# Optimization experiments

Hardware: AMD Instinct MI355X
Metric: run time of the kernel (lower is better)

The kernel has to match this reference:

```python
import jax, jax.numpy as jnp
import numpy as np

N, E, H, L = 20000, 1_280_000, 64, 4


def setup_inputs() -> dict:
    key = jax.random.key(0)
    ks = jax.random.split(key, 24)
    inputs = jax.random.normal(ks[0], (1, N, 6), jnp.float32)
    node_masks = jnp.ones((1, N), jnp.int32)
    send_edges = jax.random.randint(ks[1], (E,), 0, N)
    recv_edges = jax.random.randint(ks[2], (E,), 0, N)

    def w(k, shape, scale=None):
        s = (1.0 / np.sqrt(shape[-2])) if scale is None else scale
        return (jax.random.normal(k, shape, jnp.float32) * s)

    d = dict(
        inputs=inputs, node_masks=node_masks,
        send_edges=send_edges, recv_edges=recv_edges,
        emb_w=w(ks[3], (1, H)), emb_b=jnp.zeros((H,), jnp.float32),
        edge_w1=w(ks[4], (L, 2 * H + 1, H)), edge_b1=jnp.zeros((L, H), jnp.float32),
        edge_w2=w(ks[5], (L, H, H)), edge_b2=jnp.zeros((L, H), jnp.float32),
        node_w1=w(ks[6], (L, 2 * H, H)), node_b1=jnp.zeros((L, H), jnp.float32),
        node_w2=w(ks[7], (L, H, H)), node_b2=jnp.zeros((L, H), jnp.float32),
        coord_w1=w(ks[8], (L, H, H)), coord_b1=jnp.zeros((L, H), jnp.float32),
        coord_wout=w(ks[9], (L, H, 1), scale=0.001),  # xavier gain=0.001, no bias
        vel_w1=w(ks[10], (L, H, H)), vel_b1=jnp.zeros((L, H), jnp.float32),
        vel_w2=w(ks[11], (L, H, 1)), vel_b2=jnp.zeros((L, 1), jnp.float32),
    )
    return d


def reference(inputs, node_masks, send_edges, recv_edges,
              emb_w, emb_b, edge_w1, edge_b1, edge_w2, edge_b2,
              node_w1, node_b1, node_w2, node_b2,
              coord_w1, coord_b1, coord_wout,
              vel_w1, vel_b1, vel_w2, vel_b2):
    silu = jax.nn.silu
    # node_masks is all-ones -> node_inds = arange(N); all nodes active.
    pos, vel = jnp.split(inputs, 2, axis=-1)          # [1,N,3] each
    h = jnp.linalg.norm(vel, axis=-1, keepdims=True)  # speed -> [1,N,1]
    h = h @ emb_w + emb_b                             # [1,N,H]
    coord = pos
    n = coord.shape[1]
    counts = jax.ops.segment_sum(jnp.ones_like(recv_edges, dtype=coord.dtype),
                                 recv_edges, num_segments=n)
    inv_cnt = (1.0 / jnp.maximum(counts, 1.0))[None, :, None]
    seg = lambda e: jax.ops.segment_sum(e, recv_edges, num_segments=n)

    for l in range(L):
        # coord2radial
        cd = coord[:, send_edges] - coord[:, recv_edges]        # [1,E,3]
        radial = jnp.sum(cd * cd, -1, keepdims=True)            # [1,E,1]
        # edge_model
        ef_in = jnp.concatenate([h[:, send_edges], h[:, recv_edges], radial], -1)
        ef = silu(silu(ef_in @ edge_w1[l] + edge_b1[l]) @ edge_w2[l] + edge_b2[l])
        # coord_model
        cm = silu(ef @ coord_w1[l] + coord_b1[l]) @ coord_wout[l]  # [1,E,1]
        trans = jnp.clip(cd * cm, -100.0, 100.0)
        agg_mean = jax.vmap(seg)(trans) * inv_cnt                  # scatter_mean
        # velocity update
        v_gate = silu(h @ vel_w1[l] + vel_b1[l]) @ vel_w2[l] + vel_b2[l]
        vel = agg_mean + v_gate * vel
        coord = coord + vel
        # node_model (recurrent residual)
        agg_sum = jax.vmap(seg)(ef)                                # scatter_sum
        hn = jnp.concatenate([h, agg_sum], -1)
        h = silu(hn @ node_w1[l] + node_b1[l]) @ node_w2[l] + node_b2[l] + h

    pred = jnp.concatenate([coord, vel], -1)  # [1,N,6] == pred_all (all active)
    return pred
```

## Files before the change

kernel.cpp:

```cpp
#include <hip/hip_runtime.h>
#include <math.h>

#define N_NODES 20000
#define N_EDGES 1280000
#define NLAYERS 4
#define NTILE (N_EDGES/32)
#define TSTRIDE 68
#define SCHUNK 79

typedef short bf16x8 __attribute__((ext_vector_type(8)));
typedef float f32x4  __attribute__((ext_vector_type(4)));
typedef long long i64;
typedef unsigned short us;

__device__ __forceinline__ float silu_f(float x) {
    return x * __builtin_amdgcn_rcpf(1.0f + __expf(-x));
}

__device__ __forceinline__ us f2b(float x) {
    union { float f; unsigned u; } v; v.f = x;
    unsigned r = v.u + 0x7FFF + ((v.u >> 16) & 1);
    return (us)(r >> 16);
}
__device__ __forceinline__ float b2f(us u) {
    union { float f; unsigned u; } v; v.u = ((unsigned)u) << 16;
    return v.f;
}
__device__ __forceinline__ void split2r(float x, us& hi, us& lo) {
    hi = f2b(x);
    lo = f2b(x - b2f(hi));
}
__device__ __forceinline__ void split2f(float x, us& hi, us& lo) {
    union { float f; unsigned u; } v; v.f = x;
    hi = (us)(v.u >> 16);
    union { float f; unsigned u; } h; h.u = v.u & 0xFFFF0000u;
    union { float f; unsigned u; } r; r.f = x - h.f;
    lo = (us)(r.u >> 16);
}

__device__ __forceinline__ bf16x8 ld8(const us* p) {
    bf16x8 a;
    ((i64*)&a)[0] = *(const i64*)p;
    ((i64*)&a)[1] = *(const i64*)(p + 4);
    return a;
}

__device__ __forceinline__ void mfma3(f32x4& acc, bf16x8 ahi, bf16x8 alo,
                                      bf16x8 bhi, bf16x8 blo) {
    acc = __builtin_amdgcn_mfma_f32_16x16x32_bf16(ahi, bhi, acc, 0, 0, 0);
    acc = __builtin_amdgcn_mfma_f32_16x16x32_bf16(alo, bhi, acc, 0, 0, 0);
    acc = __builtin_amdgcn_mfma_f32_16x16x32_bf16(ahi, blo, acc, 0, 0, 0);
}

__global__ void k_init(const float* __restrict__ inp,
                       const float* __restrict__ emb_w,
                       const float* __restrict__ emb_b,
                       float* __restrict__ outv,
                       us* __restrict__ hbh, us* __restrict__ hbl) {
    int t = blockIdx.x * blockDim.x + threadIdx.x;
    int n = t >> 6, f = t & 63;
    if (n >= N_NODES) return;
    float vx = inp[n*6+3], vy = inp[n*6+4], vz = inp[n*6+5];
    float sp = sqrtf(vx*vx + vy*vy + vz*vz);
    float hv = sp * emb_w[f] + emb_b[f];
    us hi, lo; split2r(hv, hi, lo);
    hbh[t] = hi; hbl[t] = lo;
    if (f < 6) outv[n*6+f] = inp[n*6+f];
}

__global__ void k_cnt(const int* __restrict__ recv, int* __restrict__ counts) {
    int t = blockIdx.x*256 + threadIdx.x;
    if (t < N_EDGES) atomicAdd(&counts[recv[t]], 1);
}

__global__ void k_scan(const int* __restrict__ counts, int* __restrict__ rowstart,
                       int* __restrict__ cursor, int* __restrict__ tile2node) {
    __shared__ int buf[256];
    const int tid = threadIdx.x;
    const int lo = tid*SCHUNK;
    const int hi = (lo + SCHUNK < N_NODES) ? lo + SCHUNK : N_NODES;
    int s = 0;
    for (int i = lo; i < hi; ++i) s += counts[i];
    buf[tid] = s;
    __syncthreads();
    for (int off = 1; off < 256; off <<= 1) {
        int v = (tid >= off) ? buf[tid-off] : 0;
        __syncthreads();
        buf[tid] += v;
        __syncthreads();
    }
    int run = buf[tid] - s;
    for (int i = lo; i < hi; ++i) {
        rowstart[i] = run; cursor[i] = run;
        const int c = counts[i];
        for (int t = (run + 31) >> 5; t*32 < run + c; ++t) tile2node[t] = i;
        run += c;
    }
    if (tid < 20) rowstart[N_NODES + tid] = N_EDGES;
}

__global__ void k_scatter(const int* __restrict__ send, const int* __restrict__ recv,
                          int* __restrict__ cursor, us* __restrict__ sp16) {
    int t = blockIdx.x*256 + threadIdx.x;
    if (t < N_EDGES) {
        int p = atomicAdd(&cursor[recv[t]], 1);
        sp16[p] = (us)send[t];
    }
}

__global__ void k_prepw(const float* __restrict__ ew1, const float* __restrict__ ew2,
                        const float* __restrict__ cw1,
                        us* __restrict__ w1th, us* __restrict__ w1tl,
                        us* __restrict__ w2th, us* __restrict__ w2tl,
                        us* __restrict__ cw1th, us* __restrict__ cw1tl) {
    int t = blockIdx.x*256 + threadIdx.x;
    int l = t >> 14;
    int r = t & 16383;
    us hi, lo;
    if (r < 8192) {
        int n = r >> 7, k = r & 127;
        split2r(ew1[l*129*64 + k*64 + n], hi, lo);
        w1th[l*8192 + r] = hi; w1tl[l*8192 + r] = lo;
    } else if (r < 12288) {
        int rr = r - 8192; int n = rr >> 6, k = rr & 63;
        split2r(ew2[l*4096 + k*64 + n], hi, lo);
        w2th[l*4096 + n*64 + k] = hi; w2tl[l*4096 + n*64 + k] = lo;
    } else {
        int rr = r - 12288; int n = rr >> 6, k = rr & 63;
        split2r(cw1[l*4096 + k*64 + n], hi, lo);
        cw1th[l*4096 + n*64 + k] = hi; cw1tl[l*4096 + n*64 + k] = lo;
    }
}

__launch_bounds__(256, 4)
__global__ void k_recv(const us* __restrict__ hbh, const us* __restrict__ hbl,
                       const float* __restrict__ ew1,
                       const float* __restrict__ eb1,
                       float* __restrict__ R) {
    __shared__ float hs[4][64];
    const int tid = threadIdx.x;
    const int nn = tid >> 6, f = tid & 63;
    const int n = blockIdx.x*4 + nn;
    hs[nn][f] = b2f(hbh[(size_t)n*64+f]) + b2f(hbl[(size_t)n*64+f]);
    __syncthreads();
    float s = eb1[f];
    for (int k = 0; k < 64; ++k) s += hs[nn][k] * ew1[(64+k)*64 + f];
    R[(size_t)n*64+f] = s;
}

__launch_bounds__(128, 4)
__global__ void k_edge(const us* __restrict__ sp16, const int* __restrict__ rowstart,
                       const int* __restrict__ tile2node,
                       const us* __restrict__ hbh, const us* __restrict__ hbl,
                       const float* __restrict__ outv,
                       const float* __restrict__ R,
                       const us* __restrict__ w1th, const us* __restrict__ w1tl,
                       const us* __restrict__ w2th, const us* __restrict__ w2tl,
                       const us* __restrict__ cw1th, const us* __restrict__ cw1tl,
                       const float* __restrict__ ew1,
                       const float* __restrict__ eb2, const float* __restrict__ cb1,
                       const float* __restrict__ cwo,
                       float* __restrict__ aggs, float* __restrict__ aggm) {
    __shared__ us tileh[2][32*TSTRIDE];
    __shared__ us tilel[2][32*TSTRIDE];

    const int tid  = threadIdx.x;
    const int wid  = tid >> 6;
    const int lane = tid & 63;
    const int q    = lane >> 4;
    const int l15  = lane & 15;
    const int wbase = blockIdx.x*64 + wid*32;
    const int wtile = blockIdx.x*2 + wid;

    const int e0 = wbase + l15, e1 = e0 + 16;
    const int s0 = sp16[e0], s1 = sp16[e1];

    const int t2n = tile2node[wtile];
    const int wv = rowstart[t2n + 1 + l15];
    int seg0 = 0, seg1 = 0;
    #pragma unroll
    for (int i = 0; i < 16; ++i) {
        const int wi = __shfl(wv, i);
        seg0 += (e0 >= wi);
        seg1 += (e1 >= wi);
    }
    const int r0 = t2n + seg0, r1 = t2n + seg1;

    int sgrow[2][4];
    #pragma unroll
    for (int r = 0; r < 4; ++r) {
        sgrow[0][r] = __shfl(seg0, 4*q + r);
        sgrow[1][r] = __shfl(seg1, 4*q + r);
    }
    const int segA = __shfl(seg0, 0);
    const int segB = __shfl(seg1, 15);

    const float cdx0 = outv[s0*6+0]-outv[r0*6+0], cdy0 = outv[s0*6+1]-outv[r0*6+1], cdz0 = outv[s0*6+2]-outv[r0*6+2];
    const float cdx1 = outv[s1*6+0]-outv[r1*6+0], cdy1 = outv[s1*6+1]-outv[r1*6+1], cdz1 = outv[s1*6+2]-outv[r1*6+2];
    const float rad0 = cdx0*cdx0+cdy0*cdy0+cdz0*cdz0;
    const float rad1 = cdx1*cdx1+cdy1*cdy1+cdz1*cdz1;

    f32x4 acc[2][4];

    if (segB == segA) {
        const int rn = t2n + segA;
        #pragma unroll
        for (int t = 0; t < 4; ++t) {
            const float rv = R[(size_t)rn*64 + 16*t + l15];
            #pragma unroll
            for (int mu = 0; mu < 2; ++mu)
                #pragma unroll
                for (int r = 0; r < 4; ++r) acc[mu][t][r] = rv;
        }
    } else {
        #pragma unroll
        for (int mu = 0; mu < 2; ++mu)
            #pragma unroll
            for (int r = 0; r < 4; ++r) {
                const size_t ro = (size_t)(t2n + sgrow[mu][r])*64;
                #pragma unroll
                for (int t = 0; t < 4; ++t)
                    acc[mu][t][r] = R[ro + 16*t + l15];
            }
    }

    #pragma unroll
    for (int kc = 0; kc < 2; ++kc) {
        const int off = kc*32 + q*8;
        const size_t o0 = (size_t)s0*64 + off;
        const size_t o1 = (size_t)s1*64 + off;
        bf16x8 a0h = ld8(hbh + o0), a0l = ld8(hbl + o0);
        bf16x8 a1h = ld8(hbh + o1), a1l = ld8(hbl + o1);
        #pragma unroll
        for (int t = 0; t < 4; ++t) {
            const int wo = (16*t + l15)*128 + off;
            bf16x8 bh = ld8(w1th + wo), bl = ld8(w1tl + wo);
            mfma3(acc[0][t], a0h, a0l, bh, bl);
            mfma3(acc[1][t], a1h, a1l, bh, bl);
        }
    }

    float rsh0[4], rsh1[4];
    #pragma unroll
    for (int r = 0; r < 4; ++r) {
        rsh0[r] = __shfl(rad0, 4*q + r);
        rsh1[r] = __shfl(rad1, 4*q + r);
    }
    #pragma unroll
    for (int t = 0; t < 4; ++t) {
        const float wl = ew1[128*64 + 16*t + l15];
        #pragma unroll
        for (int r = 0; r < 4; ++r) {
            acc[0][t][r] += rsh0[r]*wl;
            acc[1][t][r] += rsh1[r]*wl;
        }
    }

    us* Th = tileh[wid];
    us* Tl = tilel[wid];
    #pragma unroll
    for (int mu = 0; mu < 2; ++mu)
        #pragma unroll
        for (int t = 0; t < 4; ++t)
            #pragma unroll
            for (int r = 0; r < 4; ++r) {
                us hi, lo; split2f(silu_f(acc[mu][t][r]), hi, lo);
                const int ti = (mu*16 + 4*q + r)*TSTRIDE + 16*t + l15;
                Th[ti] = hi; Tl[ti] = lo;
            }
    __asm__ volatile("s_waitcnt lgkmcnt(0)" ::: "memory");

    #pragma unroll
    for (int mu = 0; mu < 2; ++mu)
        #pragma unroll
        for (int t = 0; t < 4; ++t) acc[mu][t] = (f32x4){0.f,0.f,0.f,0.f};
    #pragma unroll
    for (int kc = 0; kc < 2; ++kc) {
        const int t0 = l15*TSTRIDE + kc*32 + q*8;
        const int t1i = (16+l15)*TSTRIDE + kc*32 + q*8;
        bf16x8 a0h = ld8(Th + t0),  a0l = ld8(Tl + t0);
        bf16x8 a1h = ld8(Th + t1i), a1l = ld8(Tl + t1i);
        #pragma unroll
        for (int t = 0; t < 4; ++t) {
            const int wo = (16*t + l15)*64 + kc*32 + q*8;
            bf16x8 bh = ld8(w2th + wo), bl = ld8(w2tl + wo);
            mfma3(acc[0][t], a0h, a0l, bh, bl);
            mfma3(acc[1][t], a1h, a1l, bh, bl);
        }
    }

    float ef[2][4][4];
    #pragma unroll
    for (int t = 0; t < 4; ++t) {
        const float bb = eb2[16*t + l15];
        #pragma unroll
        for (int mu = 0; mu < 2; ++mu)
            #pragma unroll
            for (int r = 0; r < 4; ++r)
                ef[mu][t][r] = silu_f(acc[mu][t][r] + bb);
    }
    __asm__ volatile("s_waitcnt lgkmcnt(0)" ::: "memory");
    #pragma unroll
    for (int mu = 0; mu < 2; ++mu)
        #pragma unroll
        for (int t = 0; t < 4; ++t)
            #pragma unroll
            for (int r = 0; r < 4; ++r) {
                us hi, lo; split2f(ef[mu][t][r], hi, lo);
                const int ti = (mu*16 + 4*q + r)*TSTRIDE + 16*t + l15;
                Th[ti] = hi; Tl[ti] = lo;
            }
    __asm__ volatile("s_waitcnt lgkmcnt(0)" ::: "memory");

    #pragma unroll
    for (int mu = 0; mu < 2; ++mu)
        #pragma unroll
        for (int t = 0; t < 4; ++t) acc[mu][t] = (f32x4){0.f,0.f,0.f,0.f};
    #pragma unroll
    for (int kc = 0; kc < 2; ++kc) {
        const int t0 = l15*TSTRIDE + kc*32 + q*8;
        const int t1i = (16+l15)*TSTRIDE + kc*32 + q*8;
        bf16x8 a0h = ld8(Th + t0),  a0l = ld8(Tl + t0);
        bf16x8 a1h = ld8(Th + t1i), a1l = ld8(Tl + t1i);
        #pragma unroll
        for (int t = 0; t < 4; ++t) {
            const int wo = (16*t + l15)*64 + kc*32 + q*8;
            bf16x8 bh = ld8(cw1th + wo), bl = ld8(cw1tl + wo);
            mfma3(acc[0][t], a0h, a0l, bh, bl);
            mfma3(acc[1][t], a1h, a1l, bh, bl);
        }
    }

    float cm0[4] = {0.f,0.f,0.f,0.f}, cm1[4] = {0.f,0.f,0.f,0.f};
    #pragma unroll
    for (int t = 0; t < 4; ++t) {
        const int col = 16*t + l15;
        const float cb = cb1[col];
        const float co = cwo[col];
        #pragma unroll
        for (int r = 0; r < 4; ++r) {
            cm0[r] += silu_f(acc[0][t][r] + cb) * co;
            cm1[r] += silu_f(acc[1][t][r] + cb) * co;
        }
    }
    #pragma unroll
    for (int m = 1; m <= 8; m <<= 1)
        #pragma unroll
        for (int r = 0; r < 4; ++r) {
            cm0[r] += __shfl_xor(cm0[r], m);
            cm1[r] += __shfl_xor(cm1[r], m);
        }

    float tv[2][4];
    #pragma unroll
    for (int mu = 0; mu < 2; ++mu)
        #pragma unroll
        for (int r = 0; r < 4; ++r) {
            const float cxv = __shfl(mu ? cdx1 : cdx0, 4*q + r);
            const float cyv = __shfl(mu ? cdy1 : cdy0, 4*q + r);
            const float czv = __shfl(mu ? cdz1 : cdz0, 4*q + r);
            const float cmv = mu ? cm1[r] : cm0[r];
            const float sel = (l15 == 0) ? cxv : (l15 == 1) ? cyv : czv;
            tv[mu][r] = (l15 < 3) ? fminf(fmaxf(sel*cmv, -100.f), 100.f) : 0.f;
        }

    if (segB == segA) {
        float s4[4], trT = 0.f;
        #pragma unroll
        for (int t = 0; t < 4; ++t) {
            float v = 0.f;
            #pragma unroll
            for (int mu = 0; mu < 2; ++mu)
                #pragma unroll
                for (int r = 0; r < 4; ++r) v += ef[mu][t][r];
            v += __shfl_xor(v, 16);
            v += __shfl_xor(v, 32);
            s4[t] = v;
        }
        #pragma unroll
        for (int mu = 0; mu < 2; ++mu)
            #pragma unroll
            for (int r = 0; r < 4; ++r) trT += tv[mu][r];
        trT += __shfl_xor(trT, 16);
        trT += __shfl_xor(trT, 32);
        const int rn = t2n + segA;
        if (q == 0) {
            #pragma unroll
            for (int t = 0; t < 4; ++t)
                atomicAdd(&aggs[(size_t)rn*64 + 16*t + l15], s4[t]);
            if (l15 < 3) atomicAdd(&aggm[rn*3 + l15], trT);
        }
    } else if (segB == segA + 1) {
        float sA[4] = {0,0,0,0}, sB[4] = {0,0,0,0};
        float trA = 0.f, trB = 0.f;
        #pragma unroll
        for (int mu = 0; mu < 2; ++mu)
            #pragma unroll
            for (int r = 0; r < 4; ++r) {
                const bool isA = (sgrow[mu][r] == segA);
                #pragma unroll
                for (int t = 0; t < 4; ++t) {
                    const float v = ef[mu][t][r];
                    sA[t] += isA ? v : 0.f;
                    sB[t] += isA ? 0.f : v;
                }
                const float tvv = tv[mu][r];
                trA += isA ? tvv : 0.f;
                trB += isA ? 0.f : tvv;
            }
        #pragma unroll
        for (int t = 0; t < 4; ++t) {
            sA[t] += __shfl_xor(sA[t], 16); sA[t] += __shfl_xor(sA[t], 32);
            sB[t] += __shfl_xor(sB[t], 16); sB[t] += __shfl_xor(sB[t], 32);
        }
        trA += __shfl_xor(trA, 16); trA += __shfl_xor(trA, 32);
        trB += __shfl_xor(trB, 16); trB += __shfl_xor(trB, 32);
        const int rnA = t2n + segA, rnB = rnA + 1;
        if (q == 0) {
            #pragma unroll
            for (int t = 0; t < 4; ++t) {
                atomicAdd(&aggs[(size_t)rnA*64 + 16*t + l15], sA[t]);
                atomicAdd(&aggs[(size_t)rnB*64 + 16*t + l15], sB[t]);
            }
            if (l15 < 3) {
                atomicAdd(&aggm[rnA*3 + l15], trA);
                atomicAdd(&aggm[rnB*3 + l15], trB);
            }
        }
    } else {
        #pragma unroll
        for (int mu = 0; mu < 2; ++mu)
            #pragma unroll
            for (int r = 0; r < 4; ++r) {
                const int ren = t2n + sgrow[mu][r];
                #pragma unroll
                for (int t = 0; t < 4; ++t)
                    atomicAdd(&aggs[(size_t)ren*64 + 16*t + l15], ef[mu][t][r]);
                if (l15 < 3) atomicAdd(&aggm[ren*3 + l15], tv[mu][r]);
            }
    }
}

__launch_bounds__(256, 4)
__global__ void k_node(float* __restrict__ aggs, float* __restrict__ aggm,
                       const int* __restrict__ rowstart,
                       const float* __restrict__ VW1, const float* __restrict__ vb1,
                       const float* __restrict__ VW2, const float* __restrict__ vb2,
                       const float* __restrict__ NW1, const float* __restrict__ nb1,
                       const float* __restrict__ NW2, const float* __restrict__ nb2,
                       float* __restrict__ outv,
                       us* __restrict__ hbh, us* __restrict__ hbl,
                       const float* __restrict__ EW1n,
                       const float* __restrict__ eb1n,
                       float* __restrict__ R, int doR) {
    __shared__ float hs[4][64], as[4][64], tt[4][64];
    const int tid = threadIdx.x;
    const int nn = tid >> 6, f = tid & 63;
    const int n = blockIdx.x*4 + nn;
    float hv = b2f(hbh[n*64+f]) + b2f(hbl[n*64+f]);
    hs[nn][f] = hv;
    as[nn][f] = aggs[n*64+f];
    aggs[n*64+f] = 0.f;
    __syncthreads();

    float a1 = vb1[f];
    for (int k = 0; k < 64; ++k) a1 += hs[nn][k] * VW1[k*64+f];
    float p = silu_f(a1) * VW2[f];
    #pragma unroll
    for (int o = 32; o > 0; o >>= 1) p += __shfl_down(p, o);
    float vgate = __shfl(p, 0) + vb2[0];

    if (f < 3) {
        float icnt = 1.0f / fmaxf((float)(rowstart[n+1] - rowstart[n]), 1.0f);
        float nv = aggm[n*3+f]*icnt + vgate*outv[n*6+3+f];
        aggm[n*3+f] = 0.f;
        outv[n*6+3+f] = nv;
        outv[n*6+f]  += nv;
    }

    float b = nb1[f];
    for (int k = 0; k < 64; ++k) b += hs[nn][k]*NW1[k*64+f];
    for (int k = 0; k < 64; ++k) b += as[nn][k]*NW1[(64+k)*64+f];
    __syncthreads();
    tt[nn][f] = silu_f(b);
    __syncthreads();
    float o = nb2[f] + hv;
    for (int k = 0; k < 64; ++k) o += tt[nn][k]*NW2[k*64+f];
    us hi, lo; split2r(o, hi, lo);
    hbh[n*64+f] = hi; hbl[n*64+f] = lo;

    if (doR) {
        hs[nn][f] = o;
        __syncthreads();
        float s = eb1n[f];
        for (int k = 0; k < 64; ++k) s += hs[nn][k] * EW1n[(64+k)*64 + f];
        R[(size_t)n*64+f] = s;
    }
}

extern "C" void kernel_launch(void* const* d_in, const int* in_sizes, int n_in,
                              void* d_out, int out_size, void* d_ws, size_t ws_size,
                              hipStream_t stream) {
    const float* inp   = (const float*)d_in[0];
    const int*   send  = (const int*)d_in[2];
    const int*   recv  = (const int*)d_in[3];
    const float* emb_w = (const float*)d_in[4];
    const float* emb_b = (const float*)d_in[5];
    const float* ew1   = (const float*)d_in[6];
    const float* eb1   = (const float*)d_in[7];
    const float* ew2   = (const float*)d_in[8];
    const float* eb2   = (const float*)d_in[9];
    const float* nw1   = (const float*)d_in[10];
    const float* nb1   = (const float*)d_in[11];
    const float* nw2   = (const float*)d_in[12];
    const float* nb2   = (const float*)d_in[13];
    const float* cw1   = (const float*)d_in[14];
    const float* cb1   = (const float*)d_in[15];
    const float* cwo   = (const float*)d_in[16];
    const float* vw1   = (const float*)d_in[17];
    const float* vb1   = (const float*)d_in[18];
    const float* vw2   = (const float*)d_in[19];
    const float* vb2   = (const float*)d_in[20];

    float* outv = (float*)d_out;

    float* ws        = (float*)d_ws;
    float* aggs      = ws;
    float* aggm      = aggs + (size_t)N_NODES*64;
    int*   rowstart  = (int*)(aggm + N_NODES*3);
    int*   tile2node = rowstart + (N_NODES+20);
    us*    hbh       = (us*)(tile2node + NTILE);
    us*    hbl       = hbh + (size_t)N_NODES*64;
    us*    sp16      = hbl + (size_t)N_NODES*64;
    us*    w1th      = sp16 + N_EDGES;
    us*    w1tl      = w1th + 4*8192;
    us*    w2th      = w1tl + 4*8192;
    us*    w2tl      = w2th + 4*4096;
    us*    cw1th     = w2tl + 4*4096;
    us*    cw1tl     = cw1th + 4*4096;
    float* R         = (float*)(cw1tl + 4*4096);
    int*   counts    = (int*)aggs;
    int*   cursor    = counts + N_NODES;

    hipMemsetAsync(counts, 0, N_NODES*sizeof(int), stream);
    k_init<<<(N_NODES*64)/256, 256, 0, stream>>>(inp, emb_w, emb_b, outv, hbh, hbl);
    k_cnt<<<(N_EDGES+255)/256, 256, 0, stream>>>(recv, counts);
    k_scan<<<1, 256, 0, stream>>>(counts, rowstart, cursor, tile2node);
    k_scatter<<<(N_EDGES+255)/256, 256, 0, stream>>>(send, recv, cursor, sp16);
    k_prepw<<<256, 256, 0, stream>>>(ew1, ew2, cw1, w1th, w1tl, w2th, w2tl, cw1th, cw1tl);
    hipMemsetAsync(aggs, 0, (size_t)N_NODES*67*sizeof(float), stream);
    k_recv<<<N_NODES/4, 256, 0, stream>>>(hbh, hbl, ew1, eb1, R);

    for (int l = 0; l < NLAYERS; ++l) {
        k_edge<<<N_EDGES/64, 128, 0, stream>>>(sp16, rowstart, tile2node, hbh, hbl, outv, R,
            w1th + l*8192, w1tl + l*8192,
            w2th + l*4096, w2tl + l*4096,
            cw1th + l*4096, cw1tl + l*4096,
            ew1 + (size_t)l*129*64, eb2 + l*64,
            cb1 + l*64, cwo + l*64,
            aggs, aggm);
        const int doR = (l < NLAYERS-1);
        k_node<<<N_NODES/4, 256, 0, stream>>>(aggs, aggm, rowstart,
            vw1 + (size_t)l*64*64, vb1 + l*64, vw2 + l*64, vb2 + l,
            nw1 + (size_t)l*128*64, nb1 + l*64,
            nw2 + (size_t)l*64*64,  nb2 + l*64,
            outv, hbh, hbl,
            ew1 + (size_t)(l+1 < NLAYERS ? l+1 : l)*129*64,
            eb1 + (l+1 < NLAYERS ? l+1 : l)*64,
            R, doR);
    }
}
```

Baseline: 1.777 ms.

## Swap MFMA operand roles to chain edge MLP layers in registers without LDS

```diff
diff --git a/kernel.cpp b/kernel.cpp
--- a/kernel.cpp
+++ b/kernel.cpp
@@ -5,7 +5,6 @@
 #define N_EDGES 1280000
 #define NLAYERS 4
 #define NTILE (N_EDGES/32)
-#define TSTRIDE 68
 #define SCHUNK 79
 
 typedef short bf16x8 __attribute__((ext_vector_type(8)));
@@ -43,6 +42,16 @@
     ((i64*)&a)[0] = *(const i64*)p;
     ((i64*)&a)[1] = *(const i64*)(p + 4);
     return a;
+}
+
+__device__ __forceinline__ bf16x8 pack8(us h0, us h1, us h2, us h3,
+                                        us l0, us l1, us l2, us l3) {
+    union { bf16x8 v; unsigned u[4]; } w;
+    w.u[0] = (unsigned)h0 | ((unsigned)h1 << 16);
+    w.u[1] = (unsigned)h2 | ((unsigned)h3 << 16);
+    w.u[2] = (unsigned)l0 | ((unsigned)l1 << 16);
+    w.u[3] = (unsigned)l2 | ((unsigned)l3 << 16);
+    return w.v;
 }
 
 __device__ __forceinline__ void mfma3(f32x4& acc, bf16x8 ahi, bf16x8 alo,
@@ -111,24 +120,30 @@
 __global__ void k_prepw(const float* __restrict__ ew1, const float* __restrict__ ew2,
                         const float* __restrict__ cw1,
                         us* __restrict__ w1th, us* __restrict__ w1tl,
-                        us* __restrict__ w2th, us* __restrict__ w2tl,
-                        us* __restrict__ cw1th, us* __restrict__ cw1tl) {
+                        us* __restrict__ w2a1, us* __restrict__ w2a2,
+                        us* __restrict__ cwa1, us* __restrict__ cwa2) {
     int t = blockIdx.x*256 + threadIdx.x;
-    int l = t >> 14;
-    int r = t & 16383;
+    int l = t / 24576;
+    int r = t % 24576;
     us hi, lo;
     if (r < 8192) {
         int n = r >> 7, k = r & 127;
         split2r(ew1[l*129*64 + k*64 + n], hi, lo);
         w1th[l*8192 + r] = hi; w1tl[l*8192 + r] = lo;
-    } else if (r < 12288) {
-        int rr = r - 8192; int n = rr >> 6, k = rr & 63;
-        split2r(ew2[l*4096 + k*64 + n], hi, lo);
-        w2th[l*4096 + n*64 + k] = hi; w2tl[l*4096 + n*64 + k] = lo;
+    } else if (r < 16384) {
+        int rr = r - 8192;
+        int m = rr >> 7, v = rr & 127;
+        int kt = v >> 5, qq = (v >> 3) & 3, j = v & 7;
+        int f = 16*kt + 4*qq + (j & 3);
+        split2r(ew2[l*4096 + f*64 + m], hi, lo);
+        w2a1[l*8192 + rr] = hi; w2a2[l*8192 + rr] = lo;
     } else {
-        int rr = r - 12288; int n = rr >> 6, k = rr & 63;
-        split2r(cw1[l*4096 + k*64 + n], hi, lo);
-        cw1th[l*4096 + n*64 + k] = hi; cw1tl[l*4096 + n*64 + k] = lo;
+        int rr = r - 16384;
+        int m = rr >> 7, v = rr & 127;
+        int kt = v >> 5, qq = (v >> 3) & 3, j = v & 7;
+        int f = 16*kt + 4*qq + (j & 3);
+        split2r(cw1[l*4096 + f*64 + m], hi, lo);
+        cwa1[l*8192 + rr] = hi; cwa2[l*8192 + rr] = lo;
     }
 }
 
@@ -143,9 +158,14 @@
     const int n = blockIdx.x*4 + nn;
     hs[nn][f] = b2f(hbh[(size_t)n*64+f]) + b2f(hbl[(size_t)n*64+f]);
     __syncthreads();
-    float s = eb1[f];
-    for (int k = 0; k < 64; ++k) s += hs[nn][k] * ew1[(64+k)*64 + f];
-    R[(size_t)n*64+f] = s;
+    float p0 = 0.f, p1 = 0.f, p2 = 0.f, p3 = 0.f;
+    for (int k = 0; k < 64; k += 4) {
+        p0 += hs[nn][k+0] * ew1[(64+k+0)*64 + f];
+        p1 += hs[nn][k+1] * ew1[(64+k+1)*64 + f];
+        p2 += hs[nn][k+2] * ew1[(64+k+2)*64 + f];
+        p3 += hs[nn][k+3] * ew1[(64+k+3)*64 + f];
+    }
+    R[(size_t)n*64+f] = eb1[f] + (p0+p1) + (p2+p3);
 }
 
 __launch_bounds__(128, 4)
@@ -155,20 +175,18 @@
                        const float* __restrict__ outv,
                        const float* __restrict__ R,
                        const us* __restrict__ w1th, const us* __restrict__ w1tl,
-                       const us* __restrict__ w2th, const us* __restrict__ w2tl,
-                       const us* __restrict__ cw1th, const us* __restrict__ cw1tl,
+                       const us* __restrict__ w2a1, const us* __restrict__ w2a2,
+                       const us* __restrict__ cwa1, const us* __restrict__ cwa2,
                        const float* __restrict__ ew1,
                        const float* __restrict__ eb2, const float* __restrict__ cb1,
                        const float* __restrict__ cwo,
                        float* __restrict__ aggs, float* __restrict__ aggm) {
-    __shared__ us tileh[2][32*TSTRIDE];
-    __shared__ us tilel[2][32*TSTRIDE];
-
     const int tid  = threadIdx.x;
     const int wid  = tid >> 6;
     const int lane = tid & 63;
     const int q    = lane >> 4;
     const int l15  = lane & 15;
+    const int q8   = q*8, qb = q*4;
     const int wbase = blockIdx.x*64 + wid*32;
     const int wtile = blockIdx.x*2 + wid;
 
@@ -185,13 +203,6 @@
         seg1 += (e1 >= wi);
     }
     const int r0 = t2n + seg0, r1 = t2n + seg1;
-
-    int sgrow[2][4];
-    #pragma unroll
-    for (int r = 0; r < 4; ++r) {
-        sgrow[0][r] = __shfl(seg0, 4*q + r);
-        sgrow[1][r] = __shfl(seg1, 4*q + r);
-    }
     const int segA = __shfl(seg0, 0);
     const int segB = __shfl(seg1, 15);
 
@@ -200,244 +211,217 @@
     const float rad0 = cdx0*cdx0+cdy0*cdy0+cdz0*cdz0;
     const float rad1 = cdx1*cdx1+cdy1*cdy1+cdz1*cdz1;
 
+    f32x4 wl4[4], eb24[4], cb14[4], cwo4[4];
+    #pragma unroll
+    for (int t = 0; t < 4; ++t) {
+        const int cb = 16*t + qb;
+        wl4[t]  = *(const f32x4*)&ew1[8192 + cb];
+        eb24[t] = *(const f32x4*)&eb2[cb];
+        cb14[t] = *(const f32x4*)&cb1[cb];
+        cwo4[t] = *(const f32x4*)&cwo[cb];
+    }
+
     f32x4 acc[2][4];
-
     if (segB == segA) {
         const int rn = t2n + segA;
         #pragma unroll
         for (int t = 0; t < 4; ++t) {
-            const float rv = R[(size_t)rn*64 + 16*t + l15];
-            #pragma unroll
-            for (int mu = 0; mu < 2; ++mu)
-                #pragma unroll
-                for (int r = 0; r < 4; ++r) acc[mu][t][r] = rv;
+            const f32x4 rv = *(const f32x4*)&R[(size_t)rn*64 + 16*t + qb];
+            acc[0][t] = rv; acc[1][t] = rv;
         }
     } else {
-        #pragma unroll
-        for (int mu = 0; mu < 2; ++mu)
-            #pragma unroll
-            for (int r = 0; r < 4; ++r) {
-                const size_t ro = (size_t)(t2n + sgrow[mu][r])*64;
-                #pragma unroll
-                for (int t = 0; t < 4; ++t)
-                    acc[mu][t][r] = R[ro + 16*t + l15];
-            }
+        const size_t o0 = (size_t)(t2n + seg0)*64;
+        const size_t o1 = (size_t)(t2n + seg1)*64;
+        #pragma unroll
+        for (int t = 0; t < 4; ++t) {
+            acc[0][t] = *(const f32x4*)&R[o0 + 16*t + qb];
+            acc[1][t] = *(const f32x4*)&R[o1 + 16*t + qb];
+        }
     }
 
     #pragma unroll
     for (int kc = 0; kc < 2; ++kc) {
-        const int off = kc*32 + q*8;
-        const size_t o0 = (size_t)s0*64 + off;
-        const size_t o1 = (size_t)s1*64 + off;
-        bf16x8 a0h = ld8(hbh + o0), a0l = ld8(hbl + o0);
-        bf16x8 a1h = ld8(hbh + o1), a1l = ld8(hbl + o1);
+        const int off = kc*32 + q8;
+        bf16x8 b0h = ld8(hbh + (size_t)s0*64 + off), b0l = ld8(hbl + (size_t)s0*64 + off);
+        bf16x8 b1h = ld8(hbh + (size_t)s1*64 + off), b1l = ld8(hbl + (size_t)s1*64 + off);
         #pragma unroll
         for (int t = 0; t < 4; ++t) {
             const int wo = (16*t + l15)*128 + off;
-            bf16x8 bh = ld8(w1th + wo), bl = ld8(w1tl + wo);
-            mfma3(acc[0][t], a0h, a0l, bh, bl);
-            mfma3(acc[1][t], a1h, a1l, bh, bl);
-        }
-    }
-
-    float rsh0[4], rsh1[4];
-    #pragma unroll
-    for (int r = 0; r < 4; ++r) {
-        rsh0[r] = __shfl(rad0, 4*q + r);
-        rsh1[r] = __shfl(rad1, 4*q + r);
-    }
-    #pragma unroll
-    for (int t = 0; t < 4; ++t) {
-        const float wl = ew1[128*64 + 16*t + l15];
+            bf16x8 ah = ld8(w1th + wo), al = ld8(w1tl + wo);
+            mfma3(acc[0][t], ah, al, b0h, b0l);
+            mfma3(acc[1][t], ah, al, b1h, b1l);
+        }
+    }
+
+    #pragma unroll
+    for (int t = 0; t < 4; ++t)
         #pragma unroll
         for (int r = 0; r < 4; ++r) {
-            acc[0][t][r] += rsh0[r]*wl;
-            acc[1][t][r] += rsh1[r]*wl;
-        }
-    }
-
-    us* Th = tileh[wid];
-    us* Tl = tilel[wid];
+            acc[0][t][r] += rad0 * wl4[t][r];
+            acc[1][t][r] += rad1 * wl4[t][r];
+        }
+
+    f32x4 acc2[2][4];
     #pragma unroll
     for (int mu = 0; mu < 2; ++mu)
         #pragma unroll
+        for (int t = 0; t < 4; ++t) acc2[mu][t] = (f32x4){0.f,0.f,0.f,0.f};
+    #pragma unroll
+    for (int mu = 0; mu < 2; ++mu)
+        #pragma unroll
+        for (int kt = 0; kt < 4; ++kt) {
+            us h0,h1,h2,h3,l0,l1,l2,l3;
+            split2f(silu_f(acc[mu][kt][0]), h0, l0);
+            split2f(silu_f(acc[mu][kt][1]), h1, l1);
+            split2f(silu_f(acc[mu][kt][2]), h2, l2);
+            split2f(silu_f(acc[mu][kt][3]), h3, l3);
+            const bf16x8 B = pack8(h0,h1,h2,h3, l0,l1,l2,l3);
+            #pragma unroll
+            for (int t = 0; t < 4; ++t) {
+                const int wo = (16*t + l15)*128 + kt*32 + q8;
+                bf16x8 a1 = ld8(w2a1 + wo), a2 = ld8(w2a2 + wo);
+                acc2[mu][t] = __builtin_amdgcn_mfma_f32_16x16x32_bf16(a1, B, acc2[mu][t], 0, 0, 0);
+                acc2[mu][t] = __builtin_amdgcn_mfma_f32_16x16x32_bf16(a2, B, acc2[mu][t], 0, 0, 0);
+            }
+        }
+
+    f32x4 ef[2][4];
+    #pragma unroll
+    for (int mu = 0; mu < 2; ++mu)
+        #pragma unroll
         for (int t = 0; t < 4; ++t)
             #pragma unroll
+            for (int r = 0; r < 4; ++r)
+                ef[mu][t][r] = silu_f(acc2[mu][t][r] + eb24[t][r]);
+
+    f32x4 acc3[2][4];
+    #pragma unroll
+    for (int mu = 0; mu < 2; ++mu)
+        #pragma unroll
+        for (int t = 0; t < 4; ++t) acc3[mu][t] = (f32x4){0.f,0.f,0.f,0.f};
+    #pragma unroll
+    for (int mu = 0; mu < 2; ++mu)
+        #pragma unroll
+        for (int kt = 0; kt < 4; ++kt) {
+            us h0,h1,h2,h3,l0,l1,l2,l3;
+            split2f(ef[mu][kt][0], h0, l0);
+            split2f(ef[mu][kt][1], h1, l1);
+            split2f(ef[mu][kt][2], h2, l2);
+            split2f(ef[mu][kt][3], h3, l3);
+            const bf16x8 B = pack8(h0,h1,h2,h3, l0,l1,l2,l3);
+            #pragma unroll
+            for (int t = 0; t < 4; ++t) {
+                const int wo = (16*t + l15)*128 + kt*32 + q8;
+                bf16x8 a1 = ld8(cwa1 + wo), a2 = ld8(cwa2 + wo);
+                acc3[mu][t] = __builtin_amdgcn_mfma_f32_16x16x32_bf16(a1, B, acc3[mu][t], 0, 0, 0);
+                acc3[mu][t] = __builtin_amdgcn_mfma_f32_16x16x32_bf16(a2, B, acc3[mu][t], 0, 0, 0);
+            }
+        }
+
+    float cmv0 = 0.f, cmv1 = 0.f;
+    #pragma unroll
+    for (int t = 0; t < 4; ++t)
+        #pragma unroll
+        for (int r = 0; r < 4; ++r) {
+            cmv0 += silu_f(acc3[0][t][r] + cb14[t][r]) * cwo4[t][r];
+            cmv1 += silu_f(acc3[1][t][r] + cb14[t][r]) * cwo4[t][r];
+        }
+    cmv0 += __shfl_xor(cmv0, 16); cmv0 += __shfl_xor(cmv0, 32);
+    cmv1 += __shfl_xor(cmv1, 16); cmv1 += __shfl_xor(cmv1, 32);
+
+    float tv[2][3];
+    tv[0][0] = fminf(fmaxf(cdx0*cmv0, -100.f), 100.f);
+    tv[0][1] = fminf(fmaxf(cdy0*cmv0, -100.f), 100.f);
+    tv[0][2] = fminf(fmaxf(cdz0*cmv0, -100.f), 100.f);
+    tv[1][0] = fminf(fmaxf(cdx1*cmv1, -100.f), 100.f);
+    tv[1][1] = fminf(fmaxf(cdy1*cmv1, -100.f), 100.f);
+    tv[1][2] = fminf(fmaxf(cdz1*cmv1, -100.f), 100.f);
+
+    if (segB == segA) {
+        f32x4 v[4];
+        #pragma unroll
+        for (int t = 0; t < 4; ++t) {
+            v[t] = ef[0][t] + ef[1][t];
+            #pragma unroll
             for (int r = 0; r < 4; ++r) {
-                us hi, lo; split2f(silu_f(acc[mu][t][r]), hi, lo);
-                const int ti = (mu*16 + 4*q + r)*TSTRIDE + 16*t + l15;
-                Th[ti] = hi; Tl[ti] = lo;
+                float x = v[t][r];
+                x += __shfl_xor(x, 1); x += __shfl_xor(x, 2);
+                x += __shfl_xor(x, 4); x += __shfl_xor(x, 8);
+                v[t][r] = x;
             }
-    __asm__ volatile("s_waitcnt lgkmcnt(0)" ::: "memory");
-
-    #pragma unroll
-    for (int mu = 0; mu < 2; ++mu)
-        #pragma unroll
-        for (int t = 0; t < 4; ++t) acc[mu][t] = (f32x4){0.f,0.f,0.f,0.f};
-    #pragma unroll
-    for (int kc = 0; kc < 2; ++kc) {
-        const int t0 = l15*TSTRIDE + kc*32 + q*8;
-        const int t1i = (16+l15)*TSTRIDE + kc*32 + q*8;
-        bf16x8 a0h = ld8(Th + t0),  a0l = ld8(Tl + t0);
-        bf16x8 a1h = ld8(Th + t1i), a1l = ld8(Tl + t1i);
+        }
+        float t0 = tv[0][0]+tv[1][0], t1 = tv[0][1]+tv[1][1], t2 = tv[0][2]+tv[1][2];
+        t0 += __shfl_xor(t0,1); t0 += __shfl_xor(t0,2); t0 += __shfl_xor(t0,4); t0 += __shfl_xor(t0,8);
+        t1 += __shfl_xor(t1,1); t1 += __shfl_xor(t1,2); t1 += __shfl_xor(t1,4); t1 += __shfl_xor(t1,8);
+        t2 += __shfl_xor(t2,1); t2 += __shfl_xor(t2,2); t2 += __shfl_xor(t2,4); t2 += __shfl_xor(t2,8);
+        const int rn = t2n + segA;
+        if (l15 == 0) {
+            #pragma unroll
+            for (int t = 0; t < 4; ++t)
+                #pragma unroll
+                for (int r = 0; r < 4; ++r)
+                    atomicAdd(&aggs[(size_t)rn*64 + 16*t + qb + r], v[t][r]);
+        }
+        if (q == 0 && l15 < 3) {
+            const float w = (l15 == 0) ? t0 : (l15 == 1) ? t1 : t2;
+            atomicAdd(&aggm[rn*3 + l15], w);
+        }
+    } else if (segB == segA + 1) {
+        const bool A0 = (seg0 == segA), A1 = (seg1 == segA);
+        f32x4 vA[4], vB[4];
         #pragma unroll
         for (int t = 0; t < 4; ++t) {
-            const int wo = (16*t + l15)*64 + kc*32 + q*8;
-            bf16x8 bh = ld8(w2th + wo), bl = ld8(w2tl + wo);
-            mfma3(acc[0][t], a0h, a0l, bh, bl);
-            mfma3(acc[1][t], a1h, a1l, bh, bl);
-        }
-    }
-
-    float ef[2][4][4];
-    #pragma unroll
-    for (int t = 0; t < 4; ++t) {
-        const float bb = eb2[16*t + l15];
-        #pragma unroll
-        for (int mu = 0; mu < 2; ++mu)
-            #pragma unroll
-            for (int r = 0; r < 4; ++r)
-                ef[mu][t][r] = silu_f(acc[mu][t][r] + bb);
-    }
-    __asm__ volatile("s_waitcnt lgkmcnt(0)" ::: "memory");
-    #pragma unroll
-    for (int mu = 0; mu < 2; ++mu)
+            #pragma unroll
+            for (int r = 0; r < 4; ++r) {
+                const float a = (A0 ? ef[0][t][r] : 0.f) + (A1 ? ef[1][t][r] : 0.f);
+                const float b = (A0 ? 0.f : ef[0][t][r]) + (A1 ? 0.f : ef[1][t][r]);
+                float xa = a, xb = b;
+                xa += __shfl_xor(xa,1); xa += __shfl_xor(xa,2); xa += __shfl_xor(xa,4); xa += __shfl_xor(xa,8);
+                xb += __shfl_xor(xb,1); xb += __shfl_xor(xb,2); xb += __shfl_xor(xb,4); xb += __shfl_xor(xb,8);
+                vA[t][r] = xa; vB[t][r] = xb;
+            }
+        }
+        float trA[3], trB[3];
+        #pragma unroll
+        for (int c = 0; c < 3; ++c) {
+            float a = (A0 ? tv[0][c] : 0.f) + (A1 ? tv[1][c] : 0.f);
+            float b = (A0 ? 0.f : tv[0][c]) + (A1 ? 0.f : tv[1][c]);
+            a += __shfl_xor(a,1); a += __shfl_xor(a,2); a += __shfl_xor(a,4); a += __shfl_xor(a,8);
+            b += __shfl_xor(b,1); b += __shfl_xor(b,2); b += __shfl_xor(b,4); b += __shfl_xor(b,8);
+            trA[c] = a; trB[c] = b;
+        }
+        const int rnA = t2n + segA, rnB = rnA + 1;
+        if (l15 == 0) {
+            #pragma unroll
+            for (int t = 0; t < 4; ++t)
+                #pragma unroll
+                for (int r = 0; r < 4; ++r) {
+                    atomicAdd(&aggs[(size_t)rnA*64 + 16*t + qb + r], vA[t][r]);
+                    atomicAdd(&aggs[(size_t)rnB*64 + 16*t + qb + r], vB[t][r]);
+                }
+        }
+        if (q == 0 && l15 < 3) {
+            const float wa = (l15 == 0) ? trA[0] : (l15 == 1) ? trA[1] : trA[2];
+            const float wb = (l15 == 0) ? trB[0] : (l15 == 1) ? trB[1] : trB[2];
+            atomicAdd(&aggm[rnA*3 + l15], wa);
+            atomicAdd(&aggm[rnB*3 + l15], wb);
+        }
+    } else {
+        const int n0 = t2n + seg0, n1 = t2n + seg1;
         #pragma unroll
         for (int t = 0; t < 4; ++t)
             #pragma unroll
             for (int r = 0; r < 4; ++r) {
-                us hi, lo; split2f(ef[mu][t][r], hi, lo);
-                const int ti = (mu*16 + 4*q + r)*TSTRIDE + 16*t + l15;
-                Th[ti] = hi; Tl[ti] = lo;
+                atomicAdd(&aggs[(size_t)n0*64 + 16*t + qb + r], ef[0][t][r]);
+                atomicAdd(&aggs[(size_t)n1*64 + 16*t + qb + r], ef[1][t][r]);
             }
-    __asm__ volatile("s_waitcnt lgkmcnt(0)" ::: "memory");
-
-    #pragma unroll
-    for (int mu = 0; mu < 2; ++mu)
-        #pragma unroll
-        for (int t = 0; t < 4; ++t) acc[mu][t] = (f32x4){0.f,0.f,0.f,0.f};
-    #pragma unroll
-    for (int kc = 0; kc < 2; ++kc) {
-        const int t0 = l15*TSTRIDE + kc*32 + q*8;
-        const int t1i = (16+l15)*TSTRIDE + kc*32 + q*8;
-        bf16x8 a0h = ld8(Th + t0),  a0l = ld8(Tl + t0);
-        bf16x8 a1h = ld8(Th + t1i), a1l = ld8(Tl + t1i);
-        #pragma unroll
-        for (int t = 0; t < 4; ++t) {
-            const int wo = (16*t + l15)*64 + kc*32 + q*8;
-            bf16x8 bh = ld8(cw1th + wo), bl = ld8(cw1tl + wo);
-            mfma3(acc[0][t], a0h, a0l, bh, bl);
-            mfma3(acc[1][t], a1h, a1l, bh, bl);
-        }
-    }
-
-    float cm0[4] = {0.f,0.f,0.f,0.f}, cm1[4] = {0.f,0.f,0.f,0.f};
-    #pragma unroll
-    for (int t = 0; t < 4; ++t) {
-        const int col = 16*t + l15;
-        const float cb = cb1[col];
-        const float co = cwo[col];
-        #pragma unroll
-        for (int r = 0; r < 4; ++r) {
-            cm0[r] += silu_f(acc[0][t][r] + cb) * co;
-            cm1[r] += silu_f(acc[1][t][r] + cb) * co;
-        }
-    }
-    #pragma unroll
-    for (int m = 1; m <= 8; m <<= 1)
-        #pragma unroll
-        for (int r = 0; r < 4; ++r) {
-            cm0[r] += __shfl_xor(cm0[r], m);
-            cm1[r] += __shfl_xor(cm1[r], m);
-        }
-
-    float tv[2][4];
-    #pragma unroll
-    for (int mu = 0; mu < 2; ++mu)
-        #pragma unroll
-        for (int r = 0; r < 4; ++r) {
-            const float cxv = __shfl(mu ? cdx1 : cdx0, 4*q + r);
-            const float cyv = __shfl(mu ? cdy1 : cdy0, 4*q + r);
-            const float czv = __shfl(mu ? cdz1 : cdz0, 4*q + r);
-            const float cmv = mu ? cm1[r] : cm0[r];
-            const float sel = (l15 == 0) ? cxv : (l15 == 1) ? cyv : czv;
-            tv[mu][r] = (l15 < 3) ? fminf(fmaxf(sel*cmv, -100.f), 100.f) : 0.f;
-        }
-
-    if (segB == segA) {
-        float s4[4], trT = 0.f;
-        #pragma unroll
-        for (int t = 0; t < 4; ++t) {
-            float v = 0.f;
-            #pragma unroll
-            for (int mu = 0; mu < 2; ++mu)
-                #pragma unroll
-                for (int r = 0; r < 4; ++r) v += ef[mu][t][r];
-            v += __shfl_xor(v, 16);
-            v += __shfl_xor(v, 32);
-            s4[t] = v;
-        }
-        #pragma unroll
-        for (int mu = 0; mu < 2; ++mu)
-            #pragma unroll
-            for (int r = 0; r < 4; ++r) trT += tv[mu][r];
-        trT += __shfl_xor(trT, 16);
-        trT += __shfl_xor(trT, 32);
-        const int rn = t2n + segA;
         if (q == 0) {
             #pragma unroll
-            for (int t = 0; t < 4; ++t)
-                atomicAdd(&aggs[(size_t)rn*64 + 16*t + l15], s4[t]);
-            if (l15 < 3) atomicAdd(&aggm[rn*3 + l15], trT);
-        }
-    } else if (segB == segA + 1) {
-        float sA[4] = {0,0,0,0}, sB[4] = {0,0,0,0};
-        float trA = 0.f, trB = 0.f;
-        #pragma unroll
-        for (int mu = 0; mu < 2; ++mu)
-            #pragma unroll
-            for (int r = 0; r < 4; ++r) {
-                const bool isA = (sgrow[mu][r] == segA);
-                #pragma unroll
-                for (int t = 0; t < 4; ++t) {
-                    const float v = ef[mu][t][r];
-                    sA[t] += isA ? v : 0.f;
-                    sB[t] += isA ? 0.f : v;
-                }
-                const float tvv = tv[mu][r];
-                trA += isA ? tvv : 0.f;
-                trB += isA ? 0.f : tvv;
+            for (int c = 0; c < 3; ++c) {
+                atomicAdd(&aggm[n0*3 + c], tv[0][c]);
+                atomicAdd(&aggm[n1*3 + c], tv[1][c]);
             }
-        #pragma unroll
-        for (int t = 0; t < 4; ++t) {
-            sA[t] += __shfl_xor(sA[t], 16); sA[t] += __shfl_xor(sA[t], 32);
-            sB[t] += __shfl_xor(sB[t], 16); sB[t] += __shfl_xor(sB[t], 32);
-        }
-        trA += __shfl_xor(trA, 16); trA += __shfl_xor(trA, 32);
-        trB += __shfl_xor(trB, 16); trB += __shfl_xor(trB, 32);
-        const int rnA = t2n + segA, rnB = rnA + 1;
-        if (q == 0) {
-            #pragma unroll
-            for (int t = 0; t < 4; ++t) {
-                atomicAdd(&aggs[(size_t)rnA*64 + 16*t + l15], sA[t]);
-                atomicAdd(&aggs[(size_t)rnB*64 + 16*t + l15], sB[t]);
-            }
-            if (l15 < 3) {
-                atomicAdd(&aggm[rnA*3 + l15], trA);
-                atomicAdd(&aggm[rnB*3 + l15], trB);
-            }
-        }
-    } else {
-        #pragma unroll
-        for (int mu = 0; mu < 2; ++mu)
-            #pragma unroll
-            for (int r = 0; r < 4; ++r) {
-                const int ren = t2n + sgrow[mu][r];
-                #pragma unroll
-                for (int t = 0; t < 4; ++t)
-                    atomicAdd(&aggs[(size_t)ren*64 + 16*t + l15], ef[mu][t][r]);
-                if (l15 < 3) atomicAdd(&aggm[ren*3 + l15], tv[mu][r]);
-            }
+        }
     }
 }
 
@@ -463,8 +447,15 @@
     aggs[n*64+f] = 0.f;
     __syncthreads();
 
-    float a1 = vb1[f];
-    for (int k = 0; k < 64; ++k) a1 += hs[nn][k] * VW1[k*64+f];
+    float p0, p1, p2, p3;
+    p0 = p1 = p2 = p3 = 0.f;
+    for (int k = 0; k < 64; k += 4) {
+        p0 += hs[nn][k+0] * VW1[(k+0)*64+f];
+        p1 += hs[nn][k+1] * VW1[(k+1)*64+f];
+        p2 += hs[nn][k+2] * VW1[(k+2)*64+f];
+        p3 += hs[nn][k+3] * VW1[(k+3)*64+f];
+    }
+    float a1 = vb1[f] + (p0+p1) + (p2+p3);
     float p = silu_f(a1) * VW2[f];
     #pragma unroll
     for (int o = 32; o > 0; o >>= 1) p += __shfl_down(p, o);
@@ -478,23 +469,39 @@
         outv[n*6+f]  += nv;
     }
 
-    float b = nb1[f];
-    for (int k = 0; k < 64; ++k) b += hs[nn][k]*NW1[k*64+f];
-    for (int k = 0; k < 64; ++k) b += as[nn][k]*NW1[(64+k)*64+f];
+    p0 = p1 = p2 = p3 = 0.f;
+    for (int k = 0; k < 64; k += 4) {
+        p0 += hs[nn][k+0]*NW1[(k+0)*64+f] + as[nn][k+0]*NW1[(64+k+0)*64+f];
+        p1 += hs[nn][k+1]*NW1[(k+1)*64+f] + as[nn][k+1]*NW1[(64+k+1)*64+f];
+        p2 += hs[nn][k+2]*NW1[(k+2)*64+f] + as[nn][k+2]*NW1[(64+k+2)*64+f];
+        p3 += hs[nn][k+3]*NW1[(k+3)*64+f] + as[nn][k+3]*NW1[(64+k+3)*64+f];
+    }
+    float b = nb1[f] + (p0+p1) + (p2+p3);
     __syncthreads();
     tt[nn][f] = silu_f(b);
     __syncthreads();
-    float o = nb2[f] + hv;
-    for (int k = 0; k < 64; ++k) o += tt[nn][k]*NW2[k*64+f];
+    p0 = p1 = p2 = p3 = 0.f;
+    for (int k = 0; k < 64; k += 4) {
+        p0 += tt[nn][k+0]*NW2[(k+0)*64+f];
+        p1 += tt[nn][k+1]*NW2[(k+1)*64+f];
+        p2 += tt[nn][k+2]*NW2[(k+2)*64+f];
+        p3 += tt[nn][k+3]*NW2[(k+3)*64+f];
+    }
+    float o = nb2[f] + hv + (p0+p1) + (p2+p3);
     us hi, lo; split2r(o, hi, lo);
     hbh[n*64+f] = hi; hbl[n*64+f] = lo;
 
     if (doR) {
         hs[nn][f] = o;
         __syncthreads();
-        float s = eb1n[f];
-        for (int k = 0; k < 64; ++k) s += hs[nn][k] * EW1n[(64+k)*64 + f];
-        R[(size_t)n*64+f] = s;
+        p0 = p1 = p2 = p3 = 0.f;
+        for (int k = 0; k < 64; k += 4) {
+            p0 += hs[nn][k+0] * EW1n[(64+k+0)*64 + f];
+            p1 += hs[nn][k+1] * EW1n[(64+k+1)*64 + f];
+            p2 += hs[nn][k+2] * EW1n[(64+k+2)*64 + f];
+            p3 += hs[nn][k+3] * EW1n[(64+k+3)*64 + f];
+        }
+        R[(size_t)n*64+f] = eb1n[f] + (p0+p1) + (p2+p3);
     }
 }
 
@@ -534,11 +541,11 @@
     us*    sp16      = hbl + (size_t)N_NODES*64;
     us*    w1th      = sp16 + N_EDGES;
     us*    w1tl      = w1th + 4*8192;
-    us*    w2th      = w1tl + 4*8192;
-    us*    w2tl      = w2th + 4*4096;
-    us*    cw1th     = w2tl + 4*4096;
-    us*    cw1tl     = cw1th + 4*4096;
-    float* R         = (float*)(cw1tl + 4*4096);
+    us*    w2a1      = w1tl + 4*8192;
+    us*    w2a2      = w2a1 + 4*8192;
+    us*    cwa1      = w2a2 + 4*8192;
+    us*    cwa2      = cwa1 + 4*8192;
+    float* R         = (float*)(cwa2 + 4*8192);
     int*   counts    = (int*)aggs;
     int*   cursor    = counts + N_NODES;
 
@@ -547,15 +554,15 @@
     k_cnt<<<(N_EDGES+255)/256, 256, 0, stream>>>(recv, counts);
     k_scan<<<1, 256, 0, stream>>>(counts, rowstart, cursor, tile2node);
     k_scatter<<<(N_EDGES+255)/256, 256, 0, stream>>>(send, recv, cursor, sp16);
-    k_prepw<<<256, 256, 0, stream>>>(ew1, ew2, cw1, w1th, w1tl, w2th, w2tl, cw1th, cw1tl);
+    k_prepw<<<384, 256, 0, stream>>>(ew1, ew2, cw1, w1th, w1tl, w2a1, w2a2, cwa1, cwa2);
     hipMemsetAsync(aggs, 0, (size_t)N_NODES*67*sizeof(float), stream);
     k_recv<<<N_NODES/4, 256, 0, stream>>>(hbh, hbl, ew1, eb1, R);
 
     for (int l = 0; l < NLAYERS; ++l) {
         k_edge<<<N_EDGES/64, 128, 0, stream>>>(sp16, rowstart, tile2node, hbh, hbl, outv, R,
             w1th + l*8192, w1tl + l*8192,
-            w2th + l*4096, w2tl + l*4096,
-            cw1th + l*4096, cw1tl + l*4096,
+            w2a1 + l*8192, w2a2 + l*8192,
+            cwa1 + l*8192, cwa2 + l*8192,
             ew1 + (size_t)l*129*64, eb2 + l*64,
             cb1 + l*64, cwo + l*64,
             aggs, aggm);
```

Result: slower. 2.821 ms (+58.8%).
